# Kernel tuning notes

Hardware: AMD Instinct MI355X
Metric: run time of the kernel (lower is better)

The kernel has to match this reference:

```python
import jax, jax.numpy as jnp
import numpy as np

B, S, D = 2, 2048, 1024
H, DH = 16, 64  # num_heads, attention_dim


def setup_inputs() -> dict:
    key = jax.random.key(0)
    ks = jax.random.split(key, 10)
    x = jax.random.normal(ks[0], (B, S, D), dtype=jnp.float32)
    # causal mask, broadcast over batch and heads (mask==0 -> -inf)
    mask = jnp.tril(jnp.ones((S, S), dtype=jnp.int32))[None, None]
    s = 1.0 / np.sqrt(D)
    Wq = jax.random.normal(ks[1], (D, H * DH), dtype=jnp.float32) * s
    bq = jnp.zeros((H * DH,), dtype=jnp.float32)
    Wk = jax.random.normal(ks[2], (D, H * DH), dtype=jnp.float32) * s
    bk = jnp.zeros((H * DH,), dtype=jnp.float32)
    Wv = jax.random.normal(ks[3], (D, H * DH), dtype=jnp.float32) * s
    bv = jnp.zeros((H * DH,), dtype=jnp.float32)
    Wo = jax.random.normal(ks[4], (H * DH, D), dtype=jnp.float32) * (1.0 / np.sqrt(H * DH))
    bo = jnp.zeros((D,), dtype=jnp.float32)
    return {"x": x, "mask": mask, "Wq": Wq, "bq": bq, "Wk": Wk, "bk": bk,
            "Wv": Wv, "bv": bv, "Wo": Wo, "bo": bo}


def reference(x, mask, Wq, bq, Wk, bk, Wv, bv, Wo, bo):
    b, s, _ = x.shape
    q = (x @ Wq + bq).reshape(b, s, H, DH)
    k = (x @ Wk + bk).reshape(b, s, H, DH)
    v = (x @ Wv + bv).reshape(b, s, H, DH)
    # scores: [B, H, S, S]
    scores = jnp.einsum("bshd,bthd->bhst", q, k) / jnp.sqrt(jnp.float32(DH))
    scores = jnp.where(mask == 0, -jnp.inf, scores)
    w = jax.nn.softmax(scores, axis=-1)
    attended = jnp.einsum("bhst,bthd->bshd", w, v).reshape(b, s, H * DH)
    return attended @ Wo + bo
```

## Files before the change

### kernel.cpp

```cpp
#include <hip/hip_runtime.h>
#include <hip/hip_bf16.h>

#define B_ 2
#define S_ 2048
#define D_ 1024
#define H_ 16
#define DH_ 64

typedef __attribute__((ext_vector_type(8))) short bf16x8;
typedef __attribute__((ext_vector_type(4))) float f32x4;

#define QSCALE 0.18033688011112042f

__device__ __forceinline__ int chunk_off(int qt){
  return (qt <= 19) ? 2*(qt-10) : (qt <= 29 ? 20 + 3*(qt-20) : 50 + 4*(qt-30));
}
#define CHUNKS_PER_BH 58

__device__ __forceinline__ ushort f2b(float f){
  __hip_bfloat16 h = __float2bfloat16(f);
  return *reinterpret_cast<ushort*>(&h);
}

__device__ __forceinline__ unsigned cvtpk(float lo, float hi){
  unsigned r;
  asm("v_cvt_pk_bf16_f32 %0, %1, %2" : "=v"(r) : "v"(lo), "v"(hi));
  return r;
}

__device__ __forceinline__ void gload16(const ushort* g, ushort* l){
  __builtin_amdgcn_global_load_lds((const __attribute__((address_space(1))) unsigned*)g,
                                   (__attribute__((address_space(3))) unsigned*)l, 16, 0, 0);
}

__global__ __launch_bounds__(256) void k_prep(const float* __restrict__ x, ushort* __restrict__ xb,
                                              const float* __restrict__ Wq, const float* __restrict__ Wk,
                                              const float* __restrict__ Wv, const float* __restrict__ Wo,
                                              ushort* __restrict__ WqkvT, ushort* __restrict__ WoT){
  int bid = blockIdx.x, tid = threadIdx.x;
  if (bid < 2048){
    int i = (bid*256 + tid)*8;
    float4 v0 = *(const float4*)(x + i);
    float4 v1 = *(const float4*)(x + i + 4);
    uint4 o;
    o.x = f2b(v0.x) | ((unsigned)f2b(v0.y)<<16);
    o.y = f2b(v0.z) | ((unsigned)f2b(v0.w)<<16);
    o.z = f2b(v1.x) | ((unsigned)f2b(v1.y)<<16);
    o.w = f2b(v1.z) | ((unsigned)f2b(v1.w)<<16);
    *(uint4*)(xb + i) = o;
    return;
  }
  bid -= 2048;
  const int w = bid >> 10, tb = bid & 1023;
  const float* src = (w==0)?Wq:(w==1)?Wk:(w==2)?Wv:Wo;
  ushort* dst = (w==3)?WoT : WqkvT + (size_t)w*(1024*1024);
  __shared__ float tile[32][33];
  const int bx2 = tb & 31, by2 = tb >> 5;
  const int c0 = bx2*32, r0 = by2*32;
  const int tx = tid & 31, ty = tid >> 5;
  #pragma unroll
  for (int i=0;i<4;i++)
    tile[ty + i*8][tx] = src[(size_t)(r0 + ty + i*8)*1024 + c0 + tx];
  __syncthreads();
  #pragma unroll
  for (int i=0;i<4;i++)
    dst[(size_t)(c0 + ty + i*8)*1024 + r0 + tx] = f2b(tile[tx][ty + i*8]);
}

__global__ __launch_bounds__(512, 4) void k_gemm_qkv(const ushort* __restrict__ A,
                                                     const ushort* __restrict__ BT,
                                                     const float* __restrict__ b0p,
                                                     const float* __restrict__ b1p,
                                                     const float* __restrict__ b2p,
                                                     ushort* __restrict__ Cp,
                                                     int M, int N, int K){
  __shared__ ushort As[256*64];
  __shared__ ushort Bs[128*64];
  const int tid = threadIdx.x;
  const int nbn = N >> 7;
  const int bm = blockIdx.x / nbn, bn = blockIdx.x % nbn;
  const int m0 = bm << 8, n0 = bn << 7;
  const int wave = tid >> 6, lane = tid & 63;
  const int wm = (wave >> 1) << 6, wn = (wave & 1) << 6;
  const int lr = lane & 15, lq = lane >> 4;

  f32x4 acc[4][4] = {};

  const int r0 = tid >> 3;
  const int gk = (tid & 7) ^ (r0 & 7);
  const ushort* Agb = A  + (size_t)(m0 + r0)*K + gk*8;
  const ushort* Bgb = BT + (size_t)(n0 + r0)*K + gk*8;
  const int lofs = tid*8;

  for (int kt = 0; kt < K; kt += 64){
    __syncthreads();
    #pragma unroll
    for (int j=0;j<4;j++)
      gload16(Agb + (size_t)j*64*K + kt, &As[lofs + j*4096]);
    #pragma unroll
    for (int j=0;j<2;j++)
      gload16(Bgb + (size_t)j*64*K + kt, &Bs[lofs + j*4096]);
    __syncthreads();
    #pragma unroll
    for (int kk=0;kk<2;kk++){
      bf16x8 af[4], bfr[4];
      #pragma unroll
      for (int i=0;i<4;i++){
        int ra = wm + i*16 + lr;
        af[i]  = *(bf16x8*)&As[ra*64 + (((kk*4+lq) ^ (ra & 7)) << 3)];
        int rb = wn + i*16 + lr;
        bfr[i] = *(bf16x8*)&Bs[rb*64 + (((kk*4+lq) ^ (rb & 7)) << 3)];
      }
      __builtin_amdgcn_s_setprio(1);
      #pragma unroll
      for (int mi=0;mi<4;mi++)
        #pragma unroll
        for (int ni=0;ni<4;ni++)
          acc[mi][ni] = __builtin_amdgcn_mfma_f32_16x16x32_bf16(af[mi], bfr[ni], acc[mi][ni], 0, 0, 0);
      __builtin_amdgcn_s_setprio(0);
    }
  }

  const int seg = n0 >> 10;
  const float* bp = (seg==0 ? b0p : (seg==1 ? b1p : b2p));
  #pragma unroll
  for (int mi=0;mi<4;mi++){
    #pragma unroll
    for (int ni=0;ni<4;ni++){
      int col = n0 + wn + ni*16 + lr;
      int cl = col & 1023;
      float bv = bp[cl];
      int row0 = m0 + wm + mi*16 + lq*4;
      ushort* Qb = Cp;
      if (seg == 0){
        #pragma unroll
        for (int r=0;r<4;r++)
          Qb[(size_t)(row0+r)*1024 + cl] = f2b((acc[mi][ni][r] + bv) * QSCALE);
      } else if (seg == 1){
        ushort* Kb = Qb + (4u<<20);
        #pragma unroll
        for (int r=0;r<4;r++)
          Kb[(size_t)(row0+r)*1024 + cl] = f2b(acc[mi][ni][r] + bv);
      } else {
        ushort* Vt = Qb + (8u<<20);
        int bb = row0 >> 11, srow = row0 & 2047;
        uint2 pk;
        pk.x = cvtpk(acc[mi][ni][0]+bv, acc[mi][ni][1]+bv);
        pk.y = cvtpk(acc[mi][ni][2]+bv, acc[mi][ni][3]+bv);
        *(uint2*)&Vt[((size_t)(bb*1024 + cl))*2048 + srow] = pk;
      }
    }
  }
}

__global__ __launch_bounds__(256) void k_gemm_out(const ushort* __restrict__ A,
                                                  const ushort* __restrict__ BT,
                                                  const float* __restrict__ bias,
                                                  float* __restrict__ Cp,
                                                  int M, int N, int K){
  __shared__ ushort As[128*64];
  __shared__ ushort Bs[64*64];
  const int tid = threadIdx.x;
  const int nbn = N >> 6;
  const int bm = blockIdx.x / nbn, bn = blockIdx.x % nbn;
  const int m0 = bm << 7, n0 = bn << 6;
  const int wave = tid >> 6, lane = tid & 63;
  const int wm = wave << 5;
  const int lr = lane & 15, lq = lane >> 4;

  f32x4 acc[2][4] = {};

  const ushort* Ag[4]; const ushort* Bg[2]; int lofsA[4], lofsB[2];
  #pragma unroll
  for (int j=0;j<4;j++){
    int c = tid + j*256, row = c >> 3, slot = c & 7;
    int gk2 = slot ^ (row & 7);
    Ag[j] = A + (size_t)(m0 + row)*K + gk2*8;
    lofsA[j] = c*8;
  }
  #pragma unroll
  for (int j=0;j<2;j++){
    int c = tid + j*256, row = c >> 3, slot = c & 7;
    int gk2 = slot ^ (row & 7);
    Bg[j] = BT + (size_t)(n0 + row)*K + gk2*8;
    lofsB[j] = c*8;
  }

  for (int kt = 0; kt < K; kt += 64){
    __syncthreads();
    #pragma unroll
    for (int j=0;j<4;j++)
      gload16(Ag[j] + kt, &As[lofsA[j]]);
    #pragma unroll
    for (int j=0;j<2;j++)
      gload16(Bg[j] + kt, &Bs[lofsB[j]]);
    __syncthreads();
    #pragma unroll
    for (int kk=0;kk<2;kk++){
      bf16x8 af[2], bfr[4];
      #pragma unroll
      for (int i=0;i<2;i++){
        int ra = wm + i*16 + lr;
        af[i]  = *(bf16x8*)&As[ra*64 + (((kk*4+lq) ^ (ra & 7)) << 3)];
      }
      #pragma unroll
      for (int i=0;i<4;i++){
        int rb = i*16 + lr;
        bfr[i] = *(bf16x8*)&Bs[rb*64 + (((kk*4+lq) ^ (rb & 7)) << 3)];
      }
      __builtin_amdgcn_s_setprio(1);
      #pragma unroll
      for (int mi=0;mi<2;mi++)
        #pragma unroll
        for (int ni=0;ni<4;ni++)
          acc[mi][ni] = __builtin_amdgcn_mfma_f32_16x16x32_bf16(af[mi], bfr[ni], acc[mi][ni], 0, 0, 0);
      __builtin_amdgcn_s_setprio(0);
    }
  }

  #pragma unroll
  for (int mi=0;mi<2;mi++){
    #pragma unroll
    for (int ni=0;ni<4;ni++){
      int col = n0 + ni*16 + lr;
      float bv = bias[col];
      int row0 = m0 + wm + mi*16 + lq*4;
      #pragma unroll
      for (int r=0;r<4;r++)
        Cp[(size_t)(row0+r)*N + col] = acc[mi][ni][r] + bv;
    }
  }
}

__device__ __forceinline__ bf16x8 lds_frag(const ushort* base, int row, int colbytes){
  return *(const bf16x8*)((const char*)base + row*128 + (colbytes ^ ((row & 7) << 4)));
}

__global__ __launch_bounds__(256) void k_attn_mfma(const ushort* __restrict__ Qb,
                                                   const ushort* __restrict__ Kb,
                                                   const ushort* __restrict__ Vtg,
                                                   ushort* __restrict__ Ob,
                                                   ushort* __restrict__ accPb,
                                                   float* __restrict__ lP){
  __shared__ ushort Ks[64*64];
  __shared__ ushort Vs[64*64];
  __shared__ ushort Ps[4][16*64];
  const int bid = blockIdx.x;
  const int bh = bid & 31;
  const int j = 67 - (bid >> 5);
  int qt, c, nc;
  if (j < 10)      { qt = j;                c = 0;              nc = 1; }
  else if (j < 30) { int t = j-10; qt = 10 + (t>>1); c = t & 1; nc = 2; }
  else if (j < 60) { int t = j-30; int q3 = t/3; qt = 20 + q3; c = t - 3*q3; nc = 3; }
  else             { int t = j-60; qt = 30 + (t>>2); c = t & 3; nc = 4; }
  const int t0 = c*10;
  const int NT = min(t0 + 9, qt);
  const bool diag = (NT == qt);
  const bool split = (nc > 1);
  const int h = bh & 15, b = bh >> 4;
  const int q0 = qt << 6;
  const int tid = threadIdx.x;
  const int wq = tid >> 6, lane = tid & 63;
  const int ql = lane & 15, g = lane >> 4;

  bf16x8 Qf0, Qf1;
  {
    const ushort* qp = Qb + (size_t)(b*S_ + q0 + wq*16 + ql)*1024 + h*64 + g*8;
    Qf0 = *(const bf16x8*)(qp);
    Qf1 = *(const bf16x8*)(qp + 32);
  }
  bf16x8 ones;
  #pragma unroll
  for (int i=0;i<8;i++) ones[i] = (short)0x3F80;

  f32x4 lsum = {};
  f32x4 acc[4] = {};

  const int r0c = tid >> 3, cc = tid & 7;
  const int r1c = r0c + 32;
  const int ofs0 = r0c*128 + ((cc*16) ^ ((r0c & 7) << 4));
  const int ofs1 = r1c*128 + ((cc*16) ^ ((r1c & 7) << 4));
  const ushort* Kp0 = Kb  + (size_t)(b*S_ + r0c)*1024 + h*64 + cc*8;
  const ushort* Kp1 = Kb  + (size_t)(b*S_ + r1c)*1024 + h*64 + cc*8;
  const ushort* Vp0 = Vtg + (size_t)(bh*64 + r0c)*2048 + cc*8;
  const ushort* Vp1 = Vtg + (size_t)(bh*64 + r1c)*2048 + cc*8;

  uint4 ka, kc, va, vc;
  #define ALOAD(t) { \
    ka = *(const uint4*)(Kp0 + (size_t)(t)*65536); \
    kc = *(const uint4*)(Kp1 + (size_t)(t)*65536); \
    va = *(const uint4*)(Vp0 + (t)*64); \
    vc = *(const uint4*)(Vp1 + (t)*64); }

  char* Pb = (char*)Ps + wq*2048;

  ALOAD(t0);
  for (int kt = t0; ; ++kt){
    __syncthreads();
    *(uint4*)((char*)Ks + ofs0) = ka;
    *(uint4*)((char*)Ks + ofs1) = kc;
    *(uint4*)((char*)Vs + ofs0) = va;
    *(uint4*)((char*)Vs + ofs1) = vc;
    __syncthreads();
    if (kt < NT) ALOAD(kt+1);

    f32x4 sf[4] = {};
    __builtin_amdgcn_s_setprio(1);
    #pragma unroll
    for (int ki=0; ki<4; ++ki){
      bf16x8 kf = lds_frag(Ks, ki*16 + ql, g*16);
      sf[ki] = __builtin_amdgcn_mfma_f32_16x16x32_bf16(kf, Qf0, sf[ki], 0, 0, 0);
    }
    #pragma unroll
    for (int ki=0; ki<4; ++ki){
      bf16x8 kf = lds_frag(Ks, ki*16 + ql, 64 + g*16);
      sf[ki] = __builtin_amdgcn_mfma_f32_16x16x32_bf16(kf, Qf1, sf[ki], 0, 0, 0);
    }
    __builtin_amdgcn_s_setprio(0);

    float s[16];
    #pragma unroll
    for (int ki=0; ki<4; ++ki)
      #pragma unroll
      for (int r=0; r<4; ++r)
        s[ki*4+r] = sf[ki][r];
    if (diag && kt == NT){
      const int th = q0 + wq*16 + ql - NT*64;
      #pragma unroll
      for (int ki=0; ki<4; ++ki)
        #pragma unroll
        for (int r=0; r<4; ++r)
          if (ki*16 + g*4 + r > th) s[ki*4+r] = -1e30f;
    }
    #pragma unroll
    for (int i=0; i<16; ++i) s[i] = exp2f(s[i]);

    #pragma unroll
    for (int ki=0; ki<4; ++ki){
      uint2 uu;
      uu.x = cvtpk(s[ki*4+0], s[ki*4+1]);
      uu.y = cvtpk(s[ki*4+2], s[ki*4+3]);
      *(uint2*)(Pb + ql*128 + ((ki*32 + g*8) ^ ((ql & 7) << 4))) = uu;
    }

    __builtin_amdgcn_s_setprio(1);
    #pragma unroll
    for (int ks=0; ks<2; ++ks){
      bf16x8 pf = *(const bf16x8*)(Pb + ql*128 + ((ks*64 + g*16) ^ ((ql & 7) << 4)));
      #pragma unroll
      for (int ni=0; ni<4; ++ni){
        bf16x8 vf = lds_frag(Vs, ni*16 + ql, ks*64 + g*16);
        acc[ni] = __builtin_amdgcn_mfma_f32_16x16x32_bf16(pf, vf, acc[ni], 0, 0, 0);
      }
      lsum = __builtin_amdgcn_mfma_f32_16x16x32_bf16(pf, ones, lsum, 0, 0, 0);
    }
    __builtin_amdgcn_s_setprio(0);

    if (kt == NT) break;
  }
  #undef ALOAD

  if (!split){
    ushort* Op = Ob + (size_t)(b*S_ + q0 + wq*16)*1024 + h*64;
    #pragma unroll
    for (int r=0; r<4; ++r){
      float ir = 1.0f / lsum[r];
      #pragma unroll
      for (int ni=0; ni<4; ++ni)
        Op[(size_t)(g*4 + r)*1024 + ni*16 + ql] = f2b(acc[ni][r] * ir);
    }
  } else {
    const int rbase = (bh*CHUNKS_PER_BH + chunk_off(qt) + c)*64 + wq*16;
    #pragma unroll
    for (int r=0; r<4; ++r){
      const int tr = rbase + g*4 + r;
      float ir = 1.0f / lsum[r];
      #pragma unroll
      for (int ni=0; ni<4; ++ni)
        accPb[(size_t)tr*64 + ni*16 + ql] = f2b(acc[ni][r] * ir);
      if (ql == 0) lP[tr] = lsum[r];
    }
  }
}

__global__ __launch_bounds__(256) void k_combine(const ushort* __restrict__ accPb,
                                                 const float* __restrict__ lP,
                                                 ushort* __restrict__ Ob){
  const int bid = blockIdx.x;
  const int qt = 10 + (bid >> 5), bh = bid & 31;
  const int b = bh >> 4, h = bh & 15;
  const int nc = (qt <= 19) ? 2 : (qt <= 29 ? 3 : 4);
  const int base = bh*CHUNKS_PER_BH + chunk_off(qt);
  const int row = threadIdx.x >> 2, dq = (threadIdx.x & 3) * 16;

  float w[4];
  float lt = 0.f;
  for (int i=0;i<nc;++i){ w[i] = lP[(base+i)*64 + row]; lt += w[i]; }
  float inv = 1.0f / lt;

  float o[16];
  #pragma unroll
  for (int e=0;e<16;++e) o[e] = 0.f;
  for (int i=0;i<nc;++i){
    float wi = w[i] * inv;
    const ushort* p = accPb + (size_t)((base+i)*64 + row)*64 + dq;
    uint4 a0 = *(const uint4*)p, a1 = *(const uint4*)(p + 8);
    unsigned aw[8] = {a0.x,a0.y,a0.z,a0.w,a1.x,a1.y,a1.z,a1.w};
    #pragma unroll
    for (int e=0;e<8;++e){
      o[e*2]   += wi * __uint_as_float(aw[e] << 16);
      o[e*2+1] += wi * __uint_as_float(aw[e] & 0xffff0000u);
    }
  }
  unsigned ow[8];
  #pragma unroll
  for (int e=0;e<8;++e) ow[e] = cvtpk(o[e*2], o[e*2+1]);
  ushort* op = Ob + (size_t)(b*S_ + qt*64 + row)*1024 + h*64 + dq;
  uint4 o0, o1;
  o0.x=ow[0]; o0.y=ow[1]; o0.z=ow[2]; o0.w=ow[3];
  o1.x=ow[4]; o1.y=ow[5]; o1.z=ow[6]; o1.w=ow[7];
  *(uint4*)(op)     = o0;
  *(uint4*)(op + 8) = o1;
}

extern "C" void kernel_launch(void* const* d_in, const int* in_sizes, int n_in,
                              void* d_out, int out_size, void* d_ws, size_t ws_size,
                              hipStream_t stream){
  const float* x  = (const float*)d_in[0];
  const float* Wq = (const float*)d_in[2];
  const float* bq = (const float*)d_in[3];
  const float* Wk = (const float*)d_in[4];
  const float* bk = (const float*)d_in[5];
  const float* Wv = (const float*)d_in[6];
  const float* bv = (const float*)d_in[7];
  const float* Wo = (const float*)d_in[8];
  const float* bo = (const float*)d_in[9];

  char* ws = (char*)d_ws;
  const size_t MB = 1024u*1024u;
  ushort* xb    = (ushort*)(ws + 0);
  ushort* WqkvT = (ushort*)(ws + 8*MB);
  ushort* WoT   = (ushort*)(ws + 14*MB);
  ushort* Qb    = (ushort*)(ws + 16*MB);
  ushort* Kb    = (ushort*)(ws + 24*MB);
  ushort* Vtg   = (ushort*)(ws + 32*MB);
  float*  lP    = (float*)(ws + 40*MB);
  ushort* attb  = xb;
  ushort* accPb = (ushort*)d_out;

  const int MN = B_*S_;

  k_prep<<<dim3(6144), dim3(256), 0, stream>>>(x, xb, Wq, Wk, Wv, Wo, WqkvT, WoT);

  k_gemm_qkv<<<dim3((MN/256)*(3072/128)), dim3(512), 0, stream>>>(xb, WqkvT, bq, bk, bv, Qb, MN, 3072, 1024);

  k_attn_mfma<<<dim3(2176), dim3(256), 0, stream>>>(Qb, Kb, Vtg, attb, accPb, lP);
  k_combine<<<dim3(704), dim3(256), 0, stream>>>(accPb, lP, attb);

  k_gemm_out<<<dim3((MN/128)*(1024/64)), dim3(256), 0, stream>>>(attb, WoT, bo, (float*)d_out, MN, 1024, 1024);
}
```

Measured before the change: 108.7 us.

## Load K/V MFMA fragments directly from global memory, dropping LDS staging

The attention kernel stops staging each 64x64 K and V tile into shared memory behind two block barriers. Each wave now reads its MFMA operand fragments straight from global memory (relying on L1/L2 caching), which removes the LDS writes and __syncthreads. In exchange the four waves each fetch the same K/V data redundantly, the next tile is no longer prefetched, and global load latency now sits directly before the MFMAs.

```diff
diff --git a/kernel.cpp b/kernel.cpp
--- a/kernel.cpp
+++ b/kernel.cpp
@@ -232,18 +232,12 @@
   }
 }
 
-__device__ __forceinline__ bf16x8 lds_frag(const ushort* base, int row, int colbytes){
-  return *(const bf16x8*)((const char*)base + row*128 + (colbytes ^ ((row & 7) << 4)));
-}
-
 __global__ __launch_bounds__(256) void k_attn_mfma(const ushort* __restrict__ Qb,
                                                    const ushort* __restrict__ Kb,
                                                    const ushort* __restrict__ Vtg,
                                                    ushort* __restrict__ Ob,
                                                    ushort* __restrict__ accPb,
                                                    float* __restrict__ lP){
-  __shared__ ushort Ks[64*64];
-  __shared__ ushort Vs[64*64];
   __shared__ ushort Ps[4][16*64];
   const int bid = blockIdx.x;
   const int bh = bid & 31;
@@ -276,47 +270,27 @@
   f32x4 lsum = {};
   f32x4 acc[4] = {};
 
-  const int r0c = tid >> 3, cc = tid & 7;
-  const int r1c = r0c + 32;
-  const int ofs0 = r0c*128 + ((cc*16) ^ ((r0c & 7) << 4));
-  const int ofs1 = r1c*128 + ((cc*16) ^ ((r1c & 7) << 4));
-  const ushort* Kp0 = Kb  + (size_t)(b*S_ + r0c)*1024 + h*64 + cc*8;
-  const ushort* Kp1 = Kb  + (size_t)(b*S_ + r1c)*1024 + h*64 + cc*8;
-  const ushort* Vp0 = Vtg + (size_t)(bh*64 + r0c)*2048 + cc*8;
-  const ushort* Vp1 = Vtg + (size_t)(bh*64 + r1c)*2048 + cc*8;
-
-  uint4 ka, kc, va, vc;
-  #define ALOAD(t) { \
-    ka = *(const uint4*)(Kp0 + (size_t)(t)*65536); \
-    kc = *(const uint4*)(Kp1 + (size_t)(t)*65536); \
-    va = *(const uint4*)(Vp0 + (t)*64); \
-    vc = *(const uint4*)(Vp1 + (t)*64); }
+  const ushort* Kfp = Kb  + (size_t)(b*S_ + ql)*1024 + h*64 + g*8;
+  const ushort* Vfp = Vtg + (size_t)(bh*64 + ql)*2048 + g*8;
 
   char* Pb = (char*)Ps + wq*2048;
 
-  ALOAD(t0);
   for (int kt = t0; ; ++kt){
-    __syncthreads();
-    *(uint4*)((char*)Ks + ofs0) = ka;
-    *(uint4*)((char*)Ks + ofs1) = kc;
-    *(uint4*)((char*)Vs + ofs0) = va;
-    *(uint4*)((char*)Vs + ofs1) = vc;
-    __syncthreads();
-    if (kt < NT) ALOAD(kt+1);
-
     f32x4 sf[4] = {};
-    __builtin_amdgcn_s_setprio(1);
-    #pragma unroll
-    for (int ki=0; ki<4; ++ki){
-      bf16x8 kf = lds_frag(Ks, ki*16 + ql, g*16);
-      sf[ki] = __builtin_amdgcn_mfma_f32_16x16x32_bf16(kf, Qf0, sf[ki], 0, 0, 0);
-    }
-    #pragma unroll
-    for (int ki=0; ki<4; ++ki){
-      bf16x8 kf = lds_frag(Ks, ki*16 + ql, 64 + g*16);
-      sf[ki] = __builtin_amdgcn_mfma_f32_16x16x32_bf16(kf, Qf1, sf[ki], 0, 0, 0);
-    }
-    __builtin_amdgcn_s_setprio(0);
+    #pragma unroll
+    for (int ks=0; ks<2; ++ks){
+      bf16x8 kf0 = *(const bf16x8*)(Kfp + (size_t)(kt*64 +  0)*1024 + ks*32);
+      bf16x8 kf1 = *(const bf16x8*)(Kfp + (size_t)(kt*64 + 16)*1024 + ks*32);
+      bf16x8 kf2 = *(const bf16x8*)(Kfp + (size_t)(kt*64 + 32)*1024 + ks*32);
+      bf16x8 kf3 = *(const bf16x8*)(Kfp + (size_t)(kt*64 + 48)*1024 + ks*32);
+      const bf16x8 qf = ks ? Qf1 : Qf0;
+      __builtin_amdgcn_s_setprio(1);
+      sf[0] = __builtin_amdgcn_mfma_f32_16x16x32_bf16(kf0, qf, sf[0], 0, 0, 0);
+      sf[1] = __builtin_amdgcn_mfma_f32_16x16x32_bf16(kf1, qf, sf[1], 0, 0, 0);
+      sf[2] = __builtin_amdgcn_mfma_f32_16x16x32_bf16(kf2, qf, sf[2], 0, 0, 0);
+      sf[3] = __builtin_amdgcn_mfma_f32_16x16x32_bf16(kf3, qf, sf[3], 0, 0, 0);
+      __builtin_amdgcn_s_setprio(0);
+    }
 
     float s[16];
     #pragma unroll
@@ -343,22 +317,24 @@
       *(uint2*)(Pb + ql*128 + ((ki*32 + g*8) ^ ((ql & 7) << 4))) = uu;
     }
 
-    __builtin_amdgcn_s_setprio(1);
     #pragma unroll
     for (int ks=0; ks<2; ++ks){
       bf16x8 pf = *(const bf16x8*)(Pb + ql*128 + ((ks*64 + g*16) ^ ((ql & 7) << 4)));
-      #pragma unroll
-      for (int ni=0; ni<4; ++ni){
-        bf16x8 vf = lds_frag(Vs, ni*16 + ql, ks*64 + g*16);
-        acc[ni] = __builtin_amdgcn_mfma_f32_16x16x32_bf16(pf, vf, acc[ni], 0, 0, 0);
-      }
+      bf16x8 vf0 = *(const bf16x8*)(Vfp + (size_t)( 0)*2048 + kt*64 + ks*32);
+      bf16x8 vf1 = *(const bf16x8*)(Vfp + (size_t)(16)*2048 + kt*64 + ks*32);
+      bf16x8 vf2 = *(const bf16x8*)(Vfp + (size_t)(32)*2048 + kt*64 + ks*32);
+      bf16x8 vf3 = *(const bf16x8*)(Vfp + (size_t)(48)*2048 + kt*64 + ks*32);
+      __builtin_amdgcn_s_setprio(1);
+      acc[0] = __builtin_amdgcn_mfma_f32_16x16x32_bf16(pf, vf0, acc[0], 0, 0, 0);
+      acc[1] = __builtin_amdgcn_mfma_f32_16x16x32_bf16(pf, vf1, acc[1], 0, 0, 0);
+      acc[2] = __builtin_amdgcn_mfma_f32_16x16x32_bf16(pf, vf2, acc[2], 0, 0, 0);
+      acc[3] = __builtin_amdgcn_mfma_f32_16x16x32_bf16(pf, vf3, acc[3], 0, 0, 0);
       lsum = __builtin_amdgcn_mfma_f32_16x16x32_bf16(pf, ones, lsum, 0, 0, 0);
-    }
-    __builtin_amdgcn_s_setprio(0);
+      __builtin_amdgcn_s_setprio(0);
+    }
 
     if (kt == NT) break;
   }
-  #undef ALOAD
 
   if (!split){
     ushort* Op = Ob + (size_t)(b*S_ + q0 + wq*16)*1024 + h*64;
```

After: 203.8 us. 87.5% more time.

## Double-buffer K/V tiles in LDS with one barrier per iteration

Applied to the files above, without the earlier changes.

Gives the K and V shared-memory tiles two buffers, so the next tile is written into the spare buffer while the current one is consumed, and global loads are issued two tiles ahead. The loop drops from two barriers per iteration to one. The score temporaries are also kept in the MFMA accumulator vectors instead of being copied to a scalar array. This doubles K/V LDS usage, which may lower occupancy, and holds prefetched registers live for longer.

```diff
diff --git a/kernel.cpp b/kernel.cpp
--- a/kernel.cpp
+++ b/kernel.cpp
@@ -242,8 +242,8 @@
                                                    ushort* __restrict__ Ob,
                                                    ushort* __restrict__ accPb,
                                                    float* __restrict__ lP){
-  __shared__ ushort Ks[64*64];
-  __shared__ ushort Vs[64*64];
+  __shared__ ushort Ks[2][64*64];
+  __shared__ ushort Vs[2][64*64];
   __shared__ ushort Ps[4][16*64];
   const int bid = blockIdx.x;
   const int bh = bid & 31;
@@ -291,55 +291,58 @@
     kc = *(const uint4*)(Kp1 + (size_t)(t)*65536); \
     va = *(const uint4*)(Vp0 + (t)*64); \
     vc = *(const uint4*)(Vp1 + (t)*64); }
+  #define AWRITE(buf) { \
+    *(uint4*)((char*)Ks[buf] + ofs0) = ka; \
+    *(uint4*)((char*)Ks[buf] + ofs1) = kc; \
+    *(uint4*)((char*)Vs[buf] + ofs0) = va; \
+    *(uint4*)((char*)Vs[buf] + ofs1) = vc; }
 
   char* Pb = (char*)Ps + wq*2048;
 
   ALOAD(t0);
+  AWRITE(0);
+  if (t0 + 1 <= NT) ALOAD(t0+1);
+  __syncthreads();
+  int cur = 0;
   for (int kt = t0; ; ++kt){
-    __syncthreads();
-    *(uint4*)((char*)Ks + ofs0) = ka;
-    *(uint4*)((char*)Ks + ofs1) = kc;
-    *(uint4*)((char*)Vs + ofs0) = va;
-    *(uint4*)((char*)Vs + ofs1) = vc;
-    __syncthreads();
-    if (kt < NT) ALOAD(kt+1);
+    if (kt < NT){
+      AWRITE(cur^1);
+      if (kt + 2 <= NT) ALOAD(kt+2);
+    }
 
     f32x4 sf[4] = {};
     __builtin_amdgcn_s_setprio(1);
     #pragma unroll
     for (int ki=0; ki<4; ++ki){
-      bf16x8 kf = lds_frag(Ks, ki*16 + ql, g*16);
+      bf16x8 kf = lds_frag(Ks[cur], ki*16 + ql, g*16);
       sf[ki] = __builtin_amdgcn_mfma_f32_16x16x32_bf16(kf, Qf0, sf[ki], 0, 0, 0);
     }
     #pragma unroll
     for (int ki=0; ki<4; ++ki){
-      bf16x8 kf = lds_frag(Ks, ki*16 + ql, 64 + g*16);
+      bf16x8 kf = lds_frag(Ks[cur], ki*16 + ql, 64 + g*16);
       sf[ki] = __builtin_amdgcn_mfma_f32_16x16x32_bf16(kf, Qf1, sf[ki], 0, 0, 0);
     }
     __builtin_amdgcn_s_setprio(0);
 
-    float s[16];
-    #pragma unroll
-    for (int ki=0; ki<4; ++ki)
-      #pragma unroll
-      for (int r=0; r<4; ++r)
-        s[ki*4+r] = sf[ki][r];
     if (diag && kt == NT){
       const int th = q0 + wq*16 + ql - NT*64;
       #pragma unroll
       for (int ki=0; ki<4; ++ki)
         #pragma unroll
         for (int r=0; r<4; ++r)
-          if (ki*16 + g*4 + r > th) s[ki*4+r] = -1e30f;
-    }
-    #pragma unroll
-    for (int i=0; i<16; ++i) s[i] = exp2f(s[i]);
+          if (ki*16 + g*4 + r > th) sf[ki][r] = -1e30f;
+    }
+    #pragma unroll
+    for (int ki=0; ki<4; ++ki)
+      #pragma unroll
+      for (int r=0; r<4; ++r)
+        sf[ki][r] = exp2f(sf[ki][r]);
 
     #pragma unroll
     for (int ki=0; ki<4; ++ki){
       uint2 uu;
-      uu.x = cvtpk(s[ki*4+0], s[ki*4+1]);
-      uu.y = cvtpk(s[ki*4+2], s[ki*4+3]);
+      uu.x = cvtpk(sf[ki][0], sf[ki][1]);
+      uu.y = cvtpk(sf[ki][2], sf[ki][3]);
       *(uint2*)(Pb + ql*128 + ((ki*32 + g*8) ^ ((ql & 7) << 4))) = uu;
     }
 
@@ -349,7 +352,7 @@
       bf16x8 pf = *(const bf16x8*)(Pb + ql*128 + ((ks*64 + g*16) ^ ((ql & 7) << 4)));
       #pragma unroll
       for (int ni=0; ni<4; ++ni){
-        bf16x8 vf = lds_frag(Vs, ni*16 + ql, ks*64 + g*16);
+        bf16x8 vf = lds_frag(Vs[cur], ni*16 + ql, ks*64 + g*16);
         acc[ni] = __builtin_amdgcn_mfma_f32_16x16x32_bf16(pf, vf, acc[ni], 0, 0, 0);
       }
       lsum = __builtin_amdgcn_mfma_f32_16x16x32_bf16(pf, ones, lsum, 0, 0, 0);
@@ -357,8 +360,11 @@
     __builtin_amdgcn_s_setprio(0);
 
     if (kt == NT) break;
+    __syncthreads();
+    cur ^= 1;
   }
   #undef ALOAD
+  #undef AWRITE
 
   if (!split){
     ushort* Op = Ob + (size_t)(b*S_ + q0 + wq*16)*1024 + h*64;
```

Result: no change. 109.6 us (+0.8%).
